# Kernel optimization log

Hardware: AMD Instinct MI355X
Metric: run time of the kernel (lower is better)

## Reference

```python
import jax, jax.numpy as jnp
import numpy as np
from jax import lax

B, Q, T, NC = 64, 256, 256, 256
COST_CLASS = 1.0
COST_BBOX = 1.0
MAX_DIST = 100.0
BIG = 1e9


def setup_inputs() -> dict:
    key = jax.random.key(0)
    k1, k2, k3, k4 = jax.random.split(key, 4)
    pos = jax.random.uniform(k1, (B, Q, 2), jnp.float32) * 200.0
    logits = jax.random.normal(k2, (B, Q, NC), jnp.float32)
    outputs = jnp.concatenate([pos, logits], axis=-1)  # [B,Q,2+NC]
    tgt_pos = jax.random.uniform(k3, (B, T, 2), jnp.float32) * 200.0
    tgt_ids = jax.random.randint(k4, (B, T), 0, NC, jnp.int32)
    return {"outputs": outputs, "tgt_pos": tgt_pos, "tgt_ids": tgt_ids}


def build_cost(outputs, tgt_pos, tgt_ids):
    # class distribution and position come from slices of the raw output tensor
    prob = jax.nn.softmax(outputs[..., 2:], axis=-1)  # [B,Q,NC]
    out_pos = outputs[..., :2]                        # [B,Q,2]
    # cost_class = -out_prob[:, tgt_ids] (per batch element, bs==1 in forward_)
    cost_class = -jax.vmap(lambda p, t: p[:, t])(prob, tgt_ids)  # [B,Q,T]
    # torch.cdist(out_bbox, tgt_bbox, p=2)
    d = jnp.sqrt(jnp.sum((out_pos[:, :, None, :] - tgt_pos[:, None, :, :]) ** 2, axis=-1))  # [B,Q,T]
    cost_bbox = jnp.minimum(d, MAX_DIST)                            # clamp > max_distance
    cost_bbox = jnp.where(tgt_ids[:, None, :] <= 0, MAX_DIST, cost_bbox)  # mask padded targets
    C = COST_BBOX * cost_bbox + COST_CLASS * cost_class             # [B,Q,T]
    return jnp.transpose(C, (0, 2, 1))                              # [B,T,Q]: rows=targets, cols=queries


def hungarian_square(cost):
    """Jonker-Volgenant shortest augmenting path (e-maxx variant) on a square
    [n,n] cost matrix. Returns col index assigned to each row (min total cost),
    equivalent to scipy.optimize.linear_sum_assignment up to tie-breaking."""
    n = cost.shape[0]
    NDUM = n  # dummy column used as the start of each augmenting path
    big = jnp.asarray(BIG, cost.dtype)

    def assign_row(carry, i):
        p, u, v = carry  # p[j]: row matched to col j (-1 free); u,v: potentials
        p = p.at[NDUM].set(i)
        minv = jnp.full(n + 1, big, cost.dtype)
        used = jnp.zeros(n + 1, bool)
        way = jnp.full(n + 1, NDUM, jnp.int32)

        def cond(st):
            j0, p, u, v, minv, used, way = st
            return p[j0] >= 0  # stop when we reach a free column

        def body(st):
            j0, p, u, v, minv, used, way = st
            used = used.at[j0].set(True)
            i0 = p[j0]
            cur = cost[i0] - u[i0] - v[:n]                    # reduced costs of row i0
            better = (cur < minv[:n]) & (~used[:n])
            minv = minv.at[:n].set(jnp.where(better, cur, minv[:n]))
            way = way.at[:n].set(jnp.where(better, j0, way[:n]))
            masked = jnp.where(used[:n], big, minv[:n])
            j1 = jnp.argmin(masked).astype(jnp.int32)
            delta = masked[j1]
            u = u.at[jnp.where(used, p, n)].add(jnp.where(used, delta, 0.0))
            v = jnp.where(used, v - delta, v)
            minv = jnp.where(used, minv, minv - delta)
            return (j1, p, u, v, minv, used, way)

        j0, p, u, v, minv, used, way = lax.while_loop(
            cond, body, (jnp.asarray(NDUM, jnp.int32), p, u, v, minv, used, way))

        def aug_cond(st):
            return st[0] != NDUM

        def aug_body(st):
            j0, p = st
            j1 = way[j0]
            return (j1, p.at[j0].set(p[j1]))

        _, p = lax.while_loop(aug_cond, aug_body, (j0, p))
        return (p, u, v), None

    p0 = jnp.full(n + 1, -1, jnp.int32)
    u0 = jnp.zeros(n + 1, cost.dtype)
    v0 = jnp.zeros(n + 1, cost.dtype)
    (p, _, _), _ = lax.scan(assign_row, (p0, u0, v0), jnp.arange(n, dtype=jnp.int32))
    # invert col->row into row->col
    return jnp.zeros(n, jnp.int32).at[p[:n]].set(jnp.arange(n, dtype=jnp.int32))


def reference(outputs, tgt_pos, tgt_ids):
    C = build_cost(outputs, tgt_pos, tgt_ids)       # [B,T,Q]
    cols = jax.vmap(hungarian_square)(C)            # [B,T] query index per target row
    rows = jnp.broadcast_to(jnp.arange(T, dtype=jnp.int32), (B, T))
    indices = jnp.stack([rows, cols], axis=0)       # [2,B,T], matches torch.cat(dim=1) layout
    return indices, C
```

## Files before the change

### kernel.cpp

```cpp
#include <hip/hip_runtime.h>
#include <hip/hip_bf16.h>

#define BB   64
#define QQ   256
#define TT   256
#define CD   258
#define NM   256
#define BIGF 1000000000.0f
#define WPB  8

__global__ __launch_bounds__(256) void sm_stats(const float* __restrict__ outs,
                                                float* __restrict__ rmax,
                                                float* __restrict__ rsum) {
    int row = blockIdx.x;
    int tid = threadIdx.x;
    float x = outs[(size_t)row * CD + 2 + tid];

    __shared__ float sw[5];
    float m = x;
#pragma unroll
    for (int off = 32; off; off >>= 1) m = fmaxf(m, __shfl_down(m, off, 64));
    if ((tid & 63) == 0) sw[tid >> 6] = m;
    __syncthreads();
    if (tid == 0) sw[4] = fmaxf(fmaxf(sw[0], sw[1]), fmaxf(sw[2], sw[3]));
    __syncthreads();
    float mx = sw[4];

    float s = expf(x - mx);
#pragma unroll
    for (int off = 32; off; off >>= 1) s += __shfl_down(s, off, 64);
    __syncthreads();
    if ((tid & 63) == 0) sw[tid >> 6] = s;
    __syncthreads();
    if (tid == 0) {
        rmax[row] = mx;
        rsum[row] = sw[0] + sw[1] + sw[2] + sw[3];
    }
}

__global__ __launch_bounds__(256) void build_cost(const float* __restrict__ outs,
                                                  const float* __restrict__ tpos,
                                                  const int* __restrict__ tids,
                                                  const float* __restrict__ rmax,
                                                  const float* __restrict__ rsum,
                                                  float* __restrict__ C) {
    int bt = blockIdx.x;
    int b  = bt >> 8;
    int q  = threadIdx.x;

    int   id = tids[bt];
    float tx = tpos[2 * bt];
    float ty = tpos[2 * bt + 1];

    const float* orow = outs + (size_t)(b * QQ + q) * CD;
    float dx = orow[0] - tx;
    float dy = orow[1] - ty;
    float d  = sqrtf(dx * dx + dy * dy);
    float bbox = fminf(d, 100.0f);
    if (id <= 0) bbox = 100.0f;

    int   rq  = b * QQ + q;
    float cls = expf(orow[2 + id] - rmax[rq]) / rsum[rq];

    C[(size_t)bt * QQ + q] = bbox - cls;
}

template <int CTRL, int RM>
__device__ __forceinline__ float dppmin(float x) {
    int y = __builtin_amdgcn_update_dpp(__float_as_int(x), __float_as_int(x),
                                        CTRL, RM, 0xF, false);
    return fminf(x, __int_as_float(y));
}

__global__ __launch_bounds__(64 * WPB) void jv_solve(const float* __restrict__ Call,
                                                     float* __restrict__ outIdx) {
    const int wid  = threadIdx.x >> 6;
    const int lane = threadIdx.x & 63;
    const int b    = blockIdx.x * WPB + wid;
    const float* cost = Call + (size_t)b * NM * NM;

    __shared__ float u_l[WPB][NM + 1];
    __shared__ int   p_l[WPB][NM + 1];
    __shared__ int   way_l[WPB][NM];

    float* u_s   = u_l[wid];
    int*   p_s   = p_l[wid];
    int*   way_s = way_l[wid];

    for (int k = lane; k <= NM; k += 64) {
        u_s[k] = 0.0f;
        p_s[k] = -1;
        if (k < NM) way_s[k] = NM;
    }

    float v[4] = {0.0f, 0.0f, 0.0f, 0.0f};

    for (int i = 0; i < NM; ++i) {
        float4 cr = *(const float4*)(cost + (size_t)i * NM + lane * 4);

        if (lane == 0) p_s[NM] = i;
        int   pj[4];
        float ureg[4];
#pragma unroll
        for (int s = 0; s < 4; ++s) {
            pj[s]   = p_s[lane * 4 + s];
            ureg[s] = (pj[s] >= 0) ? u_s[pj[s]] : 0.0f;
        }
        const float uof0 = ureg[0], uof1 = ureg[1], uof2 = ureg[2], uof3 = ureg[3];
        float minv[4] = {BIGF, BIGF, BIGF, BIGF};
        int   way[4]  = {NM, NM, NM, NM};
        unsigned usedm = 0;
        float ui = 0.0f;
        int   j0 = NM;
        float u0 = 0.0f;

        while (true) {
            if ((j0 >> 2) == lane) usedm |= 1u << (j0 & 3);

            float c4[4] = {cr.x, cr.y, cr.z, cr.w};
#pragma unroll
            for (int s = 0; s < 4; ++s) {
                float cur = c4[s] - u0 - v[s];
                bool  un  = !(usedm & (1u << s));
                if (un && cur < minv[s]) { minv[s] = cur; way[s] = j0; }
            }

            float cand[4];
#pragma unroll
            for (int s = 0; s < 4; ++s)
                cand[s] = (usedm & (1u << s)) ? BIGF : minv[s];
            float cA = cand[0]; int lsA = 0; int pA = pj[0]; float uA = uof0;
            if (cand[1] < cA) { cA = cand[1]; lsA = 1; pA = pj[1]; uA = uof1; }
            float cB = cand[2]; int lsB = 2; int pB = pj[2]; float uB = uof2;
            if (cand[3] < cB) { cB = cand[3]; lsB = 3; pB = pj[3]; uB = uof3; }
            if (cB < cA)      { cA = cB;      lsA = lsB; pA = pB;  uA = uB;  }

            float x = cA;
            x = dppmin<0x111, 0xF>(x);
            x = dppmin<0x112, 0xF>(x);
            x = dppmin<0x114, 0xF>(x);
            x = dppmin<0x118, 0xF>(x);
            x = dppmin<0x142, 0xA>(x);
            x = dppmin<0x143, 0xC>(x);
            float wv = __int_as_float(__builtin_amdgcn_readlane(__float_as_int(x), 63));

            unsigned long long mm = __ballot(cA == wv);
            int flane = __ffsll(mm) - 1;
            int   pk  = ((pA + 1) << 2) | lsA;
            int   wpk = __builtin_amdgcn_readlane(pk, flane);
            float u0n = __int_as_float(__builtin_amdgcn_readlane(__float_as_int(uA), flane));
            int   i0n = (wpk >> 2) - 1;
            int   j1  = flane * 4 + (wpk & 3);
            float delta = wv;

            if (i0n >= 0)
                cr = *(const float4*)(cost + (size_t)i0n * NM + lane * 4);

            ui += delta;
#pragma unroll
            for (int s = 0; s < 4; ++s) {
                if (usedm & (1u << s)) { v[s] -= delta; ureg[s] += delta; }
                else                   { minv[s] -= delta; }
            }
            j0 = j1;
            if (i0n < 0) break;
            u0 = u0n;
        }

#pragma unroll
        for (int s = 0; s < 4; ++s) {
            way_s[lane * 4 + s] = way[s];
            if (usedm & (1u << s)) u_s[pj[s]] = ureg[s];
        }
        if (lane == 0) {
            u_s[i] = ui;
            int jj = j0;
            while (jj != NM) {
                int j1w = way_s[jj];
                p_s[jj] = p_s[j1w];
                jj = j1w;
            }
        }
    }

#pragma unroll
    for (int s = 0; s < 4; ++s) {
        int j = lane * 4 + s;
        outIdx[b * TT + j] = (float)j;
        int r = p_s[j];
        outIdx[BB * TT + b * TT + r] = (float)j;
    }
}

extern "C" void kernel_launch(void* const* d_in, const int* in_sizes, int n_in,
                              void* d_out, int out_size, void* d_ws, size_t ws_size,
                              hipStream_t stream) {
    const float* outs = (const float*)d_in[0];
    const float* tpos = (const float*)d_in[1];
    const int*   tids = (const int*)d_in[2];

    float* out  = (float*)d_out;
    float* C    = out + 2 * BB * TT;
    float* rmax = (float*)d_ws;
    float* rsum = rmax + BB * QQ;

    hipLaunchKernelGGL(sm_stats,   dim3(BB * QQ), dim3(256), 0, stream, outs, rmax, rsum);
    hipLaunchKernelGGL(build_cost, dim3(BB * TT), dim3(256), 0, stream, outs, tpos, tids, rmax, rsum, C);
    hipLaunchKernelGGL(jv_solve,   dim3(BB / WPB), dim3(64 * WPB), 0, stream, C, out);
}
```

Baseline: 2.861 ms.

## Run one wave per block and stage first half of cost rows in LDS

Switches the JV solver from 8 waves per block to one wave per block, one block per batch element. It preloads the first 128 cost rows of each matrix into dynamic shared memory (128 KB) so most dependent row fetches in the augmenting loop hit LDS instead of global/L2. The latency-bound serial loop should see shorter per-step load latency. The cost is a large LDS allocation and an upfront bulk copy, and the remaining rows still come from global memory.

```diff
diff --git a/kernel.cpp b/kernel.cpp
--- a/kernel.cpp
+++ b/kernel.cpp
@@ -7,7 +7,7 @@
 #define CD   258
 #define NM   256
 #define BIGF 1000000000.0f
-#define WPB  8
+#define LROWS 128
 
 __global__ __launch_bounds__(256) void sm_stats(const float* __restrict__ outs,
                                                 float* __restrict__ rmax,
@@ -72,20 +72,22 @@
     return fminf(x, __int_as_float(y));
 }
 
-__global__ __launch_bounds__(64 * WPB) void jv_solve(const float* __restrict__ Call,
-                                                     float* __restrict__ outIdx) {
-    const int wid  = threadIdx.x >> 6;
-    const int lane = threadIdx.x & 63;
-    const int b    = blockIdx.x * WPB + wid;
+__global__ __launch_bounds__(64) void jv_solve(const float* __restrict__ Call,
+                                               float* __restrict__ outIdx) {
+    const int b    = blockIdx.x;
+    const int lane = threadIdx.x;
     const float* cost = Call + (size_t)b * NM * NM;
 
-    __shared__ float u_l[WPB][NM + 1];
-    __shared__ int   p_l[WPB][NM + 1];
-    __shared__ int   way_l[WPB][NM];
-
-    float* u_s   = u_l[wid];
-    int*   p_s   = p_l[wid];
-    int*   way_s = way_l[wid];
+    __shared__ float u_s[NM + 1];
+    __shared__ int   p_s[NM + 1];
+    __shared__ int   way_s[NM];
+    extern __shared__ float crow[];
+
+#pragma unroll 4
+    for (int r = 0; r < LROWS; ++r) {
+        float4 x = *(const float4*)(cost + (size_t)r * NM + lane * 4);
+        *(float4*)(crow + r * NM + lane * 4) = x;
+    }
 
     for (int k = lane; k <= NM; k += 64) {
         u_s[k] = 0.0f;
@@ -96,7 +98,9 @@
     float v[4] = {0.0f, 0.0f, 0.0f, 0.0f};
 
     for (int i = 0; i < NM; ++i) {
-        float4 cr = *(const float4*)(cost + (size_t)i * NM + lane * 4);
+        float4 cr;
+        if (i < LROWS) cr = *(const float4*)(crow + i * NM + lane * 4);
+        else           cr = *(const float4*)(cost + (size_t)i * NM + lane * 4);
 
         if (lane == 0) p_s[NM] = i;
         int   pj[4];
@@ -153,8 +157,10 @@
             int   j1  = flane * 4 + (wpk & 3);
             float delta = wv;
 
-            if (i0n >= 0)
-                cr = *(const float4*)(cost + (size_t)i0n * NM + lane * 4);
+            if (i0n >= 0) {
+                if (i0n < LROWS) cr = *(const float4*)(crow + i0n * NM + lane * 4);
+                else             cr = *(const float4*)(cost + (size_t)i0n * NM + lane * 4);
+            }
 
             ui += delta;
 #pragma unroll
@@ -206,5 +212,6 @@
 
     hipLaunchKernelGGL(sm_stats,   dim3(BB * QQ), dim3(256), 0, stream, outs, rmax, rsum);
     hipLaunchKernelGGL(build_cost, dim3(BB * TT), dim3(256), 0, stream, outs, tpos, tids, rmax, rsum, C);
-    hipLaunchKernelGGL(jv_solve,   dim3(BB / WPB), dim3(64 * WPB), 0, stream, C, out);
-}
+    hipLaunchKernelGGL(jv_solve,   dim3(BB),      dim3(64),
+                       LROWS * NM * sizeof(float), stream, C, out);
+}
```

After: 2.534 ms. -11.4%, faster.
